# Performance work log

Hardware: AMD Instinct MI355X
Metric: run time of the kernel (lower is better)

Reference implementation:

```python
import jax, jax.numpy as jnp
import numpy as np
import math

D_MODEL = 1024
N_HEADS = 16
D_FF = 4096
D_K = D_MODEL // N_HEADS
B, S = 2, 2048
EPS = 1e-5


def _linear_params(key, fan_in, fan_out):
    kw, kb = jax.random.split(key)
    bound = 1.0 / math.sqrt(fan_in)
    W = jax.random.uniform(kw, (fan_out, fan_in), jnp.float32, -bound, bound)
    b = jax.random.uniform(kb, (fan_out,), jnp.float32, -bound, bound)
    return W, b


def setup_inputs() -> dict:
    key = jax.random.key(0)
    ks = jax.random.split(key, 8)
    x = jax.random.normal(ks[0], (B, S, D_MODEL), jnp.float32)
    # causal mask, broadcast over batch and heads; 0 -> masked
    mask = jnp.tril(jnp.ones((S, S), jnp.int32))[None, None, :, :]
    wq, bq = _linear_params(ks[1], D_MODEL, D_MODEL)
    wk, bk = _linear_params(ks[2], D_MODEL, D_MODEL)
    wv, bv = _linear_params(ks[3], D_MODEL, D_MODEL)
    wo, bo = _linear_params(ks[4], D_MODEL, D_MODEL)
    w1, b1 = _linear_params(ks[5], D_MODEL, D_FF)
    w2, b2 = _linear_params(ks[6], D_FF, D_MODEL)
    g1 = jnp.ones((D_MODEL,), jnp.float32)
    be1 = jnp.zeros((D_MODEL,), jnp.float32)
    g2 = jnp.ones((D_MODEL,), jnp.float32)
    be2 = jnp.zeros((D_MODEL,), jnp.float32)
    return dict(x=x, mask=mask, wq=wq, bq=bq, wk=wk, bk=bk, wv=wv, bv=bv,
                wo=wo, bo=bo, w1=w1, b1=b1, w2=w2, b2=b2,
                g1=g1, be1=be1, g2=g2, be2=be2)


def _layernorm(x, g, b):
    mu = jnp.mean(x, axis=-1, keepdims=True)
    var = jnp.mean(jnp.square(x - mu), axis=-1, keepdims=True)
    return (x - mu) * jax.lax.rsqrt(var + EPS) * g + b


def reference(x, mask, wq, bq, wk, bk, wv, bv, wo, bo, w1, b1, w2, b2, g1, be1, g2, be2):
    Bsz, Sl, _ = x.shape
    def heads(t):  # [B,S,D] -> [B,H,S,d_k]
        return t.reshape(Bsz, Sl, N_HEADS, D_K).transpose(0, 2, 1, 3)
    Q = heads(x @ wq.T + bq)
    K = heads(x @ wk.T + bk)
    V = heads(x @ wv.T + bv)
    scores = jnp.einsum('bhqd,bhkd->bhqk', Q, K) / math.sqrt(D_K)
    scores = jnp.where(mask == 0, jnp.float32(-1e9), scores)
    attn = jax.nn.softmax(scores, axis=-1)
    out = jnp.einsum('bhqk,bhkd->bhqd', attn, V)
    out = out.transpose(0, 2, 1, 3).reshape(Bsz, Sl, D_MODEL)
    attn_out = out @ wo.T + bo
    h = _layernorm(x + attn_out, g1, be1)  # dropout is identity in eval
    ff = jax.nn.relu(h @ w1.T + b1) @ w2.T + b2
    return _layernorm(h + ff, g2, be2)
```

## Files before the change

kernel.cpp:

```cpp
#include <hip/hip_runtime.h>
#include <hip/hip_bf16.h>


using f32x4 = __attribute__((ext_vector_type(4))) float;
using s16x8 = __attribute__((ext_vector_type(8))) short;

constexpr int D_MODEL = 1024;
constexpr int D_FF    = 4096;
constexpr int DK      = 64;
constexpr int BB      = 2;
constexpr int SS      = 2048;
constexpr int NTOK    = BB * SS;

#define QSCALE 0.18033688011112042f

__device__ __forceinline__ ushort f2bf(float f) {
    unsigned u = __float_as_uint(f);
    u += 0x7fffu + ((u >> 16) & 1u);
    return (ushort)(u >> 16);
}

__device__ __forceinline__ float bflo(uint v) { return __uint_as_float(v << 16); }
__device__ __forceinline__ float bfhi(uint v) { return __uint_as_float(v & 0xffff0000u); }

__device__ __forceinline__ float ex2(float x) {
    float r;
    asm("v_exp_f32 %0, %1" : "=v"(r) : "v"(x));
    return r;
}

__device__ __forceinline__ void gload_lds16(const void* g, void* l) {
    __builtin_amdgcn_global_load_lds(
        (const __attribute__((address_space(1))) void*)g,
        (__attribute__((address_space(3))) void*)l, 16, 0, 0);
}

__device__ __forceinline__ void wait_vm4() {
    asm volatile("s_waitcnt vmcnt(4)" ::: "memory");
    __builtin_amdgcn_sched_barrier(0);
}
__device__ __forceinline__ void wait_vm0() {
    asm volatile("s_waitcnt vmcnt(0)" ::: "memory");
    __builtin_amdgcn_sched_barrier(0);
}
__device__ __forceinline__ void wait_lgkm0() {
    asm volatile("s_waitcnt lgkmcnt(0)" ::: "memory");
    __builtin_amdgcn_sched_barrier(0);
}

struct CvtArgs { const float* src[7]; ushort* dst[7]; };

__global__ __launch_bounds__(256) void cvt_all(CvtArgs a) {
    constexpr long S[8] = {0L<<20, 1L<<20, 2L<<20, 3L<<20,
                           4L<<20, 8L<<20, 12L<<20, 16L<<20};
    long i = ((long)blockIdx.x * 256 + threadIdx.x) * 4;
    int s = 0;
#pragma unroll
    for (int j = 1; j < 7; ++j) if (i >= S[j]) s = j;
    long off = i - S[s];
    float4 v = *(const float4*)(a.src[s] + off);
    ushort4 o;
    o.x = f2bf(v.x); o.y = f2bf(v.y); o.z = f2bf(v.z); o.w = f2bf(v.w);
    *(ushort4*)(a.dst[s] + off) = o;
}

__global__ __launch_bounds__(512, 2) void gemm256_relu(
        const ushort* __restrict__ A, const ushort* __restrict__ Wt,
        const float* __restrict__ bias, ushort* __restrict__ C,
        int M, int N, int K) {
    __shared__ __align__(16) char Als[2][2][128 * 128];
    __shared__ __align__(16) char Bls[2][2][128 * 128];

    const int nwg = (int)gridDim.x;
    const int id  = (int)blockIdx.x;
    const int sw  = (id & 7) * (nwg >> 3) + (id >> 3);
    const int gx  = N >> 8;
    const int bx  = sw % gx, by = sw / gx;
    const int bm0 = by << 8, bn0 = bx << 8;

    const int t  = threadIdx.x;
    const int l  = t & 63;
    const int w  = t >> 6;
    const int li = l & 15, g = l >> 4;
    const int wm = w >> 2, wn = w & 3;

    const int srow  = w * 8 + (l >> 3);
    const int scolb = (l & 7) * 16;
    const int svz   = (scolb ^ ((srow & 4) << 3)) >> 1;
    const int nk    = K >> 6;

    auto stA = [&](int buf, int half, int kt) {
        if (kt >= nk) return;
        const ushort* src = A + (size_t)(bm0 + half * 128 + srow) * K + kt * 64 + svz;
        char* dst = Als[buf][half] + w * 1024;
        gload_lds16(src, dst);
        gload_lds16(src + (size_t)64 * K, dst + 8192);
    };
    auto stB = [&](int buf, int half, int kt) {
        if (kt >= nk) return;
        const ushort* src = Wt + (size_t)(bn0 + half * 128 + srow) * K + kt * 64 + svz;
        char* dst = Bls[buf][half] + w * 1024;
        gload_lds16(src, dst);
        gload_lds16(src + (size_t)64 * K, dst + 8192);
    };

    const int rdsw = (li & 4) << 3;

    f32x4 acc[8][4];
#pragma unroll
    for (int m = 0; m < 8; ++m)
#pragma unroll
        for (int n = 0; n < 4; ++n)
            acc[m][n] = (f32x4){0.f, 0.f, 0.f, 0.f};

    auto ldA2 = [&](int buf, int q, s16x8 af[2][2]) {
#pragma unroll
        for (int m2 = 0; m2 < 2; ++m2)
#pragma unroll
            for (int kk = 0; kk < 2; ++kk)
                af[m2][kk] = *(const s16x8*)(Als[buf][wm] +
                    ((q * 2 + m2) * 16 + li) * 128 + ((kk * 64 + g * 16) ^ rdsw));
    };
    auto ldB8 = [&](int buf, s16x8 bfr[4][2]) {
#pragma unroll
        for (int nf = 0; nf < 4; ++nf)
#pragma unroll
            for (int kk = 0; kk < 2; ++kk)
                bfr[nf][kk] = *(const s16x8*)(Bls[buf][wn >> 1] +
                    ((wn & 1) * 64 + nf * 16 + li) * 128 + ((kk * 64 + g * 16) ^ rdsw));
    };
    auto mfmaq = [&](int q, s16x8 af[2][2], s16x8 bfr[4][2], int wm_mode) {
        __builtin_amdgcn_s_barrier();
        wait_lgkm0();
        __builtin_amdgcn_s_setprio(1);
#pragma unroll
        for (int m2 = 0; m2 < 2; ++m2)
#pragma unroll
            for (int nf = 0; nf < 4; ++nf)
#pragma unroll
            for (int kk = 0; kk < 2; ++kk)
                acc[q * 2 + m2][nf] = __builtin_amdgcn_mfma_f32_16x16x32_bf16(
                    af[m2][kk], bfr[nf][kk], acc[q * 2 + m2][nf], 0, 0, 0);
        __builtin_amdgcn_s_setprio(0);
        if (wm_mode == 4) wait_vm4();
        else if (wm_mode == 0) wait_vm0();
        __builtin_amdgcn_s_barrier();
    };

    stB(0, 0, 0); stB(0, 1, 0);
    stA(0, 0, 0); stA(0, 1, 0);
    stB(1, 0, 1); stB(1, 1, 1);
    wait_vm4();
    __builtin_amdgcn_s_barrier();

    const int ni = nk >> 1;
    for (int i = 0; i < ni; ++i) {
        const int t0 = 2 * i;
        const bool last = (i == ni - 1);
        {
            s16x8 bfr[4][2];
            { ldB8(0, bfr); s16x8 af[2][2]; ldA2(0, 0, af);
              stA(1, 0, t0 + 1);                      mfmaq(0, af, bfr, -1); }
            { s16x8 af[2][2]; ldA2(0, 1, af);
              stA(1, 1, t0 + 1); stB(0, 0, t0 + 2);   mfmaq(1, af, bfr, -1); }
            { s16x8 af[2][2]; ldA2(0, 2, af);
              stB(0, 1, t0 + 2);                      mfmaq(2, af, bfr, -1); }
            { s16x8 af[2][2]; ldA2(0, 3, af);
                                                      mfmaq(3, af, bfr, last ? 0 : 4); }
        }
        {
            s16x8 bfr[4][2];
            { ldB8(1, bfr); s16x8 af[2][2]; ldA2(1, 0, af);
              stA(0, 0, t0 + 2);                      mfmaq(0, af, bfr, -1); }
            { s16x8 af[2][2]; ldA2(1, 1, af);
              stA(0, 1, t0 + 2);                      mfmaq(1, af, bfr, -1); }
            { s16x8 af[2][2]; ldA2(1, 2, af);
              stB(1, 0, t0 + 3);                      mfmaq(2, af, bfr, -1); }
            { s16x8 af[2][2]; ldA2(1, 3, af);
              stB(1, 1, t0 + 3);
                                                      mfmaq(3, af, bfr, last ? -1 : 4); }
        }
    }

#pragma unroll
    for (int mf = 0; mf < 8; ++mf) {
        int row0 = bm0 + wm * 128 + mf * 16 + g * 4;
#pragma unroll
        for (int nf = 0; nf < 4; ++nf) {
            int col = bn0 + wn * 64 + nf * 16 + li;
            float bsv = bias[col];
#pragma unroll
            for (int r = 0; r < 4; ++r) {
                float v = fmaxf(acc[mf][nf][r] + bsv, 0.f);
                C[(size_t)(row0 + r) * N + col] = f2bf(v);
            }
        }
    }
}

template <bool RELU, bool OUTBF16>
__global__ __launch_bounds__(256, 2) void gemm_bt(
        const ushort* __restrict__ A, const ushort* __restrict__ W,
        const float* __restrict__ bias,
        void* __restrict__ Cout, int M, int N, int Klen, int ldk, int gx, int splitk) {
    __shared__ __align__(16) char Asb[2][128 * 128];
    __shared__ __align__(16) char Bsb[2][128 * 128];

    const int nwg = (int)gridDim.x;
    const int id  = (int)blockIdx.x;
    const int sw  = (id & 7) * (nwg >> 3) + (id >> 3);
    const int tps = nwg / splitk;
    const int s   = sw / tps;
    const int rem = sw - s * tps;
    const int bx  = rem % gx, by = rem / gx;

    const int t  = threadIdx.x;
    const int l  = t & 63;
    const int w  = t >> 6;
    const int wr = w >> 1, wc = w & 1;
    const int li = l & 15, g = l >> 4;
    const int bm0 = by << 7;
    const int bn0 = bx << 7;
    const int kbase = s * Klen;

    f32x4 acc[4][4];
#pragma unroll
    for (int m = 0; m < 4; ++m)
#pragma unroll
        for (int n = 0; n < 4; ++n)
            acc[m][n] = (f32x4){0.f, 0.f, 0.f, 0.f};

    const int rsub = l >> 3, slot = l & 7;
    const int swzel = (((slot * 16) ^ (rsub << 4)) >> 1);

    auto stage = [&](int buf, int k0) {
#pragma unroll
        for (int i = 0; i < 4; ++i) {
            const int rbase = i * 32 + w * 8;
            gload_lds16(A + (size_t)(bm0 + rbase + rsub) * ldk + kbase + k0 + swzel,
                        Asb[buf] + rbase * 128);
            gload_lds16(W + (size_t)(bn0 + rbase + rsub) * ldk + kbase + k0 + swzel,
                        Bsb[buf] + rbase * 128);
        }
    };

    const int nk = Klen >> 6;
    stage(0, 0);
    __syncthreads();

    for (int tt = 0; tt < nk; ++tt) {
        const int cur = tt & 1;
        if (tt + 1 < nk) stage(cur ^ 1, (tt + 1) << 6);
#pragma unroll
        for (int ks = 0; ks < 2; ++ks) {
            s16x8 af[4], bfr[4];
#pragma unroll
            for (int m = 0; m < 4; ++m) {
                int row = wr * 64 + m * 16 + li;
                af[m] = *(const s16x8*)(Asb[cur] + row * 128 + (((ks * 4 + g) * 16) ^ ((row & 7) << 4)));
            }
#pragma unroll
            for (int n = 0; n < 4; ++n) {
                int row = wc * 64 + n * 16 + li;
                bfr[n] = *(const s16x8*)(Bsb[cur] + row * 128 + (((ks * 4 + g) * 16) ^ ((row & 7) << 4)));
            }
            __builtin_amdgcn_s_setprio(1);
#pragma unroll
            for (int m = 0; m < 4; ++m)
#pragma unroll
                for (int n = 0; n < 4; ++n)
                    acc[m][n] = __builtin_amdgcn_mfma_f32_16x16x32_bf16(af[m], bfr[n], acc[m][n], 0, 0, 0);
            __builtin_amdgcn_s_setprio(0);
        }
        __syncthreads();
    }

    const bool dobias = (s == 0);
    float* Cf = (float*)Cout + (size_t)s * M * N;
#pragma unroll
    for (int m = 0; m < 4; ++m) {
        int row0 = bm0 + wr * 64 + m * 16 + g * 4;
#pragma unroll
        for (int n = 0; n < 4; ++n) {
            int col = bn0 + wc * 64 + n * 16 + li;
            float bsv = dobias ? bias[col] : 0.f;
#pragma unroll
            for (int r = 0; r < 4; ++r) {
                float v = acc[m][n][r] + bsv;
                if (RELU) v = fmaxf(v, 0.f);
                size_t idx = (size_t)(row0 + r) * N + col;
                if (OUTBF16) ((ushort*)Cout)[idx] = f2bf(v);
                else         Cf[idx] = v;
            }
        }
    }
}

__global__ __launch_bounds__(256, 2) void gemm_qkvt(
        const ushort* __restrict__ xb, const ushort* __restrict__ wqkb,
        const ushort* __restrict__ wvb,
        const float* __restrict__ bq, const float* __restrict__ bk,
        const float* __restrict__ bv,
        ushort* __restrict__ QKb, ushort* __restrict__ VtG) {
    __shared__ __align__(16) char Asb[2][128 * 128];
    __shared__ __align__(16) char Bsb[2][128 * 128];

    const int id = (int)blockIdx.x;
    const int sw = (id & 7) * 96 + (id >> 3);
    const bool vt = (sw >= 512);
    int bx, by, N;
    const ushort *A, *W;
    if (!vt) { bx = sw % 16;          by = sw / 16;          A = xb;  W = wqkb; N = 2048; }
    else     { int s2 = sw - 512; bx = s2 % 32; by = s2 / 32; A = wvb; W = xb;  N = 4096; }

    const int t  = threadIdx.x;
    const int l  = t & 63;
    const int w  = t >> 6;
    const int wr = w >> 1, wc = w & 1;
    const int li = l & 15, g = l >> 4;
    const int bm0 = by << 7;
    const int bn0 = bx << 7;

    f32x4 acc[4][4];
#pragma unroll
    for (int m = 0; m < 4; ++m)
#pragma unroll
        for (int n = 0; n < 4; ++n)
            acc[m][n] = (f32x4){0.f, 0.f, 0.f, 0.f};

    const int rsub = l >> 3, slot = l & 7;
    const int swzel = (((slot * 16) ^ (rsub << 4)) >> 1);

    auto stage = [&](int buf, int k0) {
#pragma unroll
        for (int i = 0; i < 4; ++i) {
            const int rbase = i * 32 + w * 8;
            gload_lds16(A + (size_t)(bm0 + rbase + rsub) * 1024 + k0 + swzel,
                        Asb[buf] + rbase * 128);
            gload_lds16(W + (size_t)(bn0 + rbase + rsub) * 1024 + k0 + swzel,
                        Bsb[buf] + rbase * 128);
        }
    };

    stage(0, 0);
    __syncthreads();

    for (int tt = 0; tt < 16; ++tt) {
        const int cur = tt & 1;
        if (tt + 1 < 16) stage(cur ^ 1, (tt + 1) << 6);
#pragma unroll
        for (int ks = 0; ks < 2; ++ks) {
            s16x8 af[4], bfr[4];
#pragma unroll
            for (int m = 0; m < 4; ++m) {
                int row = wr * 64 + m * 16 + li;
                af[m] = *(const s16x8*)(Asb[cur] + row * 128 + (((ks * 4 + g) * 16) ^ ((row & 7) << 4)));
            }
#pragma unroll
            for (int n = 0; n < 4; ++n) {
                int row = wc * 64 + n * 16 + li;
                bfr[n] = *(const s16x8*)(Bsb[cur] + row * 128 + (((ks * 4 + g) * 16) ^ ((row & 7) << 4)));
            }
            __builtin_amdgcn_s_setprio(1);
#pragma unroll
            for (int m = 0; m < 4; ++m)
#pragma unroll
                for (int n = 0; n < 4; ++n)
                    acc[m][n] = __builtin_amdgcn_mfma_f32_16x16x32_bf16(af[m], bfr[n], acc[m][n], 0, 0, 0);
            __builtin_amdgcn_s_setprio(0);
        }
        __syncthreads();
    }

#pragma unroll
    for (int m = 0; m < 4; ++m) {
        int row0 = bm0 + wr * 64 + m * 16 + g * 4;
#pragma unroll
        for (int n = 0; n < 4; ++n) {
            int col = bn0 + wc * 64 + n * 16 + li;
            if (!vt) {
                float bsv = (col < 1024) ? bq[col] : bk[col - 1024];
                float sc  = (col < 1024) ? QSCALE : 1.f;
#pragma unroll
                for (int r = 0; r < 4; ++r) {
                    float v = (acc[m][n][r] + bsv) * sc;
                    QKb[(size_t)(row0 + r) * 2048 + col] = f2bf(v);
                }
            } else {
#pragma unroll
                for (int r = 0; r < 4; ++r) {
                    float v = acc[m][n][r] + bv[row0 + r];
                    VtG[(size_t)(row0 + r) * 4096 + col] = f2bf(v);
                }
            }
        }
    }
}

__global__ __launch_bounds__(256, 4) void attn_kernel(
        const ushort* __restrict__ QKb, const ushort* __restrict__ VtG,
        ushort* __restrict__ po, float* __restrict__ ml) {
    __shared__ __align__(16) char Ks[2][64 * 128];
    __shared__ __align__(16) char Vs[2][64 * 128];
    __shared__ __align__(16) char Ps[4][16 * 128];

    const int t  = threadIdx.x;
    const int l  = t & 63;
    const int w  = t >> 6;
    const int li = l & 15, g = l >> 4;

    const int id   = (int)blockIdx.x;
    const int xcd  = id & 7;
    const int rest = id >> 3;
    const int grp  = xcd + 8 * (rest >> 5);
    const int k32  = rest & 31;
    const int h    = grp >> 1;
    const int b    = grp & 1;
    const int bx   = k32 & 15;
    const int half = k32 >> 4;

    const ushort* Kp = QKb + (size_t)(b * SS) * 2048 + 1024 + h * DK;
    const ushort* Vp = VtG + (size_t)(h * DK) * NTOK + b * SS;

    const int rsub = l >> 3, slot = l & 7;
    const int swzsrc = (slot * 16) ^ (rsub << 4);

    auto stage = [&](int buf, int kt) {
#pragma unroll
        for (int c = 0; c < 2; ++c) {
            int row0 = (w + c * 4) * 8;
            gload_lds16((const char*)(Kp + (size_t)(kt + row0 + rsub) * 2048) + swzsrc,
                        Ks[buf] + row0 * 128);
            gload_lds16((const char*)(Vp + (size_t)(row0 + rsub) * NTOK + kt) + swzsrc,
                        Vs[buf] + row0 * 128);
        }
    };

    char* Pw = Ps[w];
    const int rswz = (li & 7) << 4;

    const int hi  = SS / 64 - 1 - bx;
    const int lo  = bx;
    const int qwH = hi * 64 + w * 16;
    const int qwL = lo * 64 + w * 16;

    s16x8 qfH[2], qfL[2];
    {
        const ushort* QpH = QKb + (size_t)(b * SS + qwH) * 2048 + h * DK;
        const ushort* QpL = QKb + (size_t)(b * SS + qwL) * 2048 + h * DK;
#pragma unroll
        for (int ds = 0; ds < 2; ++ds) {
            qfH[ds] = *(const s16x8*)(QpH + li * 2048 + ds * 32 + g * 8);
            qfL[ds] = *(const s16x8*)(QpL + li * 2048 + ds * 32 + g * 8);
        }
    }

    f32x4 oH[4], oL[4];
#pragma unroll
    for (int d = 0; d < 4; ++d) {
        oH[d] = (f32x4){0.f, 0.f, 0.f, 0.f};
        oL[d] = (f32x4){0.f, 0.f, 0.f, 0.f};
    }
    float mH = -1e30f, lsH = 0.f, mL = -1e30f, lsL = 0.f;

    auto process = [&](const s16x8 (&qf)[2], f32x4 (&o)[4], float& m_, float& ls,
                       int j, int stripe, int qw, int cur) {
        const int kt = j * 64;
        f32x4 sa[4];
#pragma unroll
        for (int ks = 0; ks < 4; ++ks) sa[ks] = (f32x4){0.f, 0.f, 0.f, 0.f};
#pragma unroll
        for (int ks = 0; ks < 4; ++ks) {
            int row = ks * 16 + li;
#pragma unroll
            for (int ds = 0; ds < 2; ++ds) {
                s16x8 kf = *(const s16x8*)(Ks[cur] + row * 128 + ((ds * 64 + g * 16) ^ rswz));
                __builtin_amdgcn_s_setprio(1);
                sa[ks] = __builtin_amdgcn_mfma_f32_16x16x32_bf16(kf, qf[ds], sa[ks], 0, 0, 0);
                __builtin_amdgcn_s_setprio(0);
            }
        }

        const bool maskt = (j == stripe);
        float p[4][4];
        float pmax = -1e30f;
#pragma unroll
        for (int ks = 0; ks < 4; ++ks)
#pragma unroll
            for (int r = 0; r < 4; ++r) {
                float sv = sa[ks][r];
                if (maskt && (kt + ks * 16 + g * 4 + r > qw + li)) sv = -1e30f;
                p[ks][r] = sv;
                pmax = fmaxf(pmax, sv);
            }

        if (!__all(pmax <= m_ + 11.5f)) {
            float mx = fmaxf(pmax, __shfl_xor(pmax, 16));
            mx = fmaxf(mx, __shfl_xor(mx, 32));
            float nm = fmaxf(m_, mx);
            float fs = ex2(m_ - nm);
            m_ = nm;
            ls *= fs;
            float fsr[4];
#pragma unroll
            for (int r = 0; r < 4; ++r) fsr[r] = __shfl(fs, g * 4 + r);
#pragma unroll
            for (int d = 0; d < 4; ++d)
#pragma unroll
                for (int r = 0; r < 4; ++r) o[d][r] *= fsr[r];
        }
        float rs = 0.f;
#pragma unroll
        for (int ks = 0; ks < 4; ++ks)
#pragma unroll
            for (int r = 0; r < 4; ++r) {
                p[ks][r] = ex2(p[ks][r] - m_);
                rs += p[ks][r];
            }
        rs += __shfl_xor(rs, 16);
        rs += __shfl_xor(rs, 32);
        ls += rs;

#pragma unroll
        for (int ks = 0; ks < 4; ++ks) {
            uint u0, u1;
            asm("v_cvt_pk_bf16_f32 %0, %1, %2" : "=v"(u0) : "v"(p[ks][0]), "v"(p[ks][1]));
            asm("v_cvt_pk_bf16_f32 %0, %1, %2" : "=v"(u1) : "v"(p[ks][2]), "v"(p[ks][3]));
            uint2 uv; uv.x = u0; uv.y = u1;
            *(uint2*)(Pw + li * 128 + ((ks * 32 + g * 8) ^ rswz)) = uv;
        }

        s16x8 pf[2];
#pragma unroll
        for (int ks2 = 0; ks2 < 2; ++ks2)
            pf[ks2] = *(const s16x8*)(Pw + li * 128 + ((ks2 * 64 + g * 16) ^ rswz));
#pragma unroll
        for (int dblk = 0; dblk < 4; ++dblk) {
            int vrow = dblk * 16 + li;
#pragma unroll
            for (int ks2 = 0; ks2 < 2; ++ks2) {
                s16x8 vf = *(const s16x8*)(Vs[cur] + vrow * 128 + ((ks2 * 64 + g * 16) ^ rswz));
                __builtin_amdgcn_s_setprio(1);
                o[dblk] = __builtin_amdgcn_mfma_f32_16x16x32_bf16(pf[ks2], vf, o[dblk], 0, 0, 0);
                __builtin_amdgcn_s_setprio(0);
            }
        }
    };

    const int nt = ((hi - half) >> 1) + 1;
    stage(0, half * 64);
    __syncthreads();

    for (int it = 0; it < nt; ++it) {
        const int j   = half + 2 * it;
        const int cur = it & 1;
        if (it + 1 < nt) stage(cur ^ 1, j * 64 + 128);

        process(qfH, oH, mH, lsH, j, hi, qwH, cur);
        if (j <= lo)
            process(qfL, oL, mL, lsL, j, lo, qwL, cur);

        __syncthreads();
    }

#pragma unroll
    for (int r = 0; r < 4; ++r) {
        ushort* ppH = po + ((((size_t)(half * 2 + b)) * SS + qwH + g * 4 + r) * 16 + h) * 64;
        ushort* ppL = po + ((((size_t)(half * 2 + b)) * SS + qwL + g * 4 + r) * 16 + h) * 64;
#pragma unroll
        for (int dblk = 0; dblk < 4; ++dblk) {
            ppH[dblk * 16 + li] = f2bf(oH[dblk][r]);
            ppL[dblk * 16 + li] = f2bf(oL[dblk][r]);
        }
    }
    if (l < 16) {
        size_t mrowH = (((size_t)(half * 2 + b)) * SS + qwH + l) * 16 + h;
        ml[mrowH * 2]     = mH;
        ml[mrowH * 2 + 1] = lsH;
        size_t mrowL = (((size_t)(half * 2 + b)) * SS + qwL + l) * 16 + h;
        ml[mrowL * 2]     = mL;
        ml[mrowL * 2 + 1] = lsL;
    }
}

__global__ __launch_bounds__(256) void attn_combine(
        const ushort* __restrict__ po, const float* __restrict__ ml,
        ushort* __restrict__ ctx) {
    const int idx = blockIdx.x * 256 + threadIdx.x;
    const int row = idx >> 4;
    const int d4  = (idx & 15) * 4;
    const int HR  = 2 * SS * 16;

    float m0 = ml[(size_t)row * 2],        l0 = ml[(size_t)row * 2 + 1];
    float m1 = ml[(size_t)(HR + row) * 2], l1 = ml[(size_t)(HR + row) * 2 + 1];
    float mx = fmaxf(m0, m1);
    float w0 = ex2(m0 - mx), w1 = ex2(m1 - mx);
    float inv = 1.0f / (l0 * w0 + l1 * w1);

    uint2 a = *(const uint2*)(po + (size_t)row * 64 + d4);
    uint2 c = *(const uint2*)(po + (size_t)(HR + row) * 64 + d4);
    float v0 = (bflo(a.x) * w0 + bflo(c.x) * w1) * inv;
    float v1 = (bfhi(a.x) * w0 + bfhi(c.x) * w1) * inv;
    float v2 = (bflo(a.y) * w0 + bflo(c.y) * w1) * inv;
    float v3 = (bfhi(a.y) * w0 + bfhi(c.y) * w1) * inv;
    ushort4 o;
    o.x = f2bf(v0); o.y = f2bf(v1); o.z = f2bf(v2); o.w = f2bf(v3);
    *(ushort4*)(ctx + (size_t)(row >> 4) * 1024 + (row & 15) * 64 + d4) = o;
}

template <bool WBF, bool X3>
__global__ __launch_bounds__(256) void ln_fused(
        const float* __restrict__ xa, const float* __restrict__ xb,
        const float* __restrict__ xc,
        const float* __restrict__ gamma, const float* __restrict__ beta,
        float* __restrict__ outf, ushort* __restrict__ outb) {
    const int row = blockIdx.x;
    const int t   = threadIdx.x;
    const size_t off = (size_t)row * D_MODEL + t * 4;
    float4 a = *(const float4*)(xa + off);
    float4 c = *(const float4*)(xb + off);
    float z0 = a.x + c.x, z1 = a.y + c.y, z2 = a.z + c.z, z3 = a.w + c.w;
    if constexpr (X3) {
        float4 d = *(const float4*)(xc + off);
        z0 += d.x; z1 += d.y; z2 += d.z; z3 += d.w;
    }
    float sum = z0 + z1 + z2 + z3;
    float sq  = z0 * z0 + z1 * z1 + z2 * z2 + z3 * z3;
#pragma unroll
    for (int o = 1; o < 64; o <<= 1) {
        sum += __shfl_xor(sum, o);
        sq  += __shfl_xor(sq, o);
    }
    __shared__ float s1[4], s2[4];
    if ((t & 63) == 0) { s1[t >> 6] = sum; s2[t >> 6] = sq; }
    __syncthreads();
    float tot = s1[0] + s1[1] + s1[2] + s1[3];
    float tsq = s2[0] + s2[1] + s2[2] + s2[3];
    const float invn = 1.0f / (float)D_MODEL;
    float mu  = tot * invn;
    float var = tsq * invn - mu * mu;
    float rstd = rsqrtf(var + 1e-5f);
    float4 gv = *(const float4*)(gamma + t * 4);
    float4 bv = *(const float4*)(beta + t * 4);
    float y0 = (z0 - mu) * rstd * gv.x + bv.x;
    float y1 = (z1 - mu) * rstd * gv.y + bv.y;
    float y2 = (z2 - mu) * rstd * gv.z + bv.z;
    float y3 = (z3 - mu) * rstd * gv.w + bv.w;
    float4 y = {y0, y1, y2, y3};
    *(float4*)(outf + off) = y;
    if constexpr (WBF) {
        ushort4 u;
        u.x = f2bf(y0); u.y = f2bf(y1); u.z = f2bf(y2); u.w = f2bf(y3);
        *(ushort4*)(outb + off) = u;
    }
}

extern "C" void kernel_launch(void* const* d_in, const int* in_sizes, int n_in,
                              void* d_out, int out_size, void* d_ws, size_t ws_size,
                              hipStream_t stream) {
    const float* x   = (const float*)d_in[0];
    const float* wq  = (const float*)d_in[2];  const float* bq  = (const float*)d_in[3];
    const float* wk  = (const float*)d_in[4];  const float* bk  = (const float*)d_in[5];
    const float* wv  = (const float*)d_in[6];  const float* bv  = (const float*)d_in[7];
    const float* wo  = (const float*)d_in[8];  const float* bo  = (const float*)d_in[9];
    const float* w1  = (const float*)d_in[10]; const float* b1  = (const float*)d_in[11];
    const float* w2  = (const float*)d_in[12]; const float* b2  = (const float*)d_in[13];
    const float* g1  = (const float*)d_in[14]; const float* be1 = (const float*)d_in[15];
    const float* g2  = (const float*)d_in[16]; const float* be2 = (const float*)d_in[17];
    float* out = (float*)d_out;

    char* ws = (char*)d_ws;
    const size_t MB = 1u << 20;
    ushort* wqkb = (ushort*)(ws + 0 * MB);
    ushort* wvb  = (ushort*)(ws + 4 * MB);
    ushort* wob  = (ushort*)(ws + 6 * MB);
    ushort* w1b  = (ushort*)(ws + 8 * MB);
    ushort* w2b  = (ushort*)(ws + 16 * MB);
    ushort* xb   = (ushort*)(ws + 24 * MB);
    ushort* QKb  = (ushort*)(ws + 32 * MB);
    ushort* VtG  = (ushort*)(ws + 48 * MB);
    ushort* ctx  = (ushort*)(ws + 56 * MB);
    ushort* po   = (ushort*)(ws + 64 * MB);
    float*  ml   = (float*)(ws + 81 * MB);
    float*  p0   = (float*)(ws + 64 * MB);
    float*  p1   = (float*)(ws + 80 * MB);
    float*  h    = (float*)(ws + 96 * MB);
    ushort* hb   = (ushort*)(ws + 112 * MB);
    ushort* ffib = (ushort*)(ws + 24 * MB);

    CvtArgs ca;
    ca.src[0] = wq; ca.dst[0] = wqkb;
    ca.src[1] = wk; ca.dst[1] = wqkb + D_MODEL * D_MODEL;
    ca.src[2] = wv; ca.dst[2] = wvb;
    ca.src[3] = wo; ca.dst[3] = wob;
    ca.src[4] = w1; ca.dst[4] = w1b;
    ca.src[5] = w2; ca.dst[5] = w2b;
    ca.src[6] = x;  ca.dst[6] = xb;
    cvt_all<<<dim3(16384), dim3(256), 0, stream>>>(ca);

    dim3 blk(256);
    gemm_qkvt<<<dim3(768), blk, 0, stream>>>(xb, wqkb, wvb, bq, bk, bv, QKb, VtG);

    attn_kernel<<<dim3(1024), blk, 0, stream>>>(QKb, VtG, po, ml);
    attn_combine<<<dim3(4096), blk, 0, stream>>>(po, ml, ctx);

    gemm_bt<false, false><<<dim3(512), blk, 0, stream>>>(
        ctx, wob, bo, p0, NTOK, D_MODEL, 512, D_MODEL, 8, 2);
    ln_fused<true, true><<<dim3(NTOK), blk, 0, stream>>>(x, p0, p1, g1, be1, h, hb);

    gemm256_relu<<<dim3(256), dim3(512), 0, stream>>>(hb, w1b, b1, ffib, NTOK, D_FF, D_MODEL);

    gemm_bt<false, false><<<dim3(512), blk, 0, stream>>>(
        ffib, w2b, b2, p0, NTOK, D_MODEL, 2048, D_FF, 8, 2);
    ln_fused<false, true><<<dim3(NTOK), blk, 0, stream>>>(h, p0, p1, g2, be2, out, nullptr);
}
```

Before: 229.8 us.

## Replace QKV projection GEMM with 256x256-tile pipelined 8-wave kernel

The fused Q/K/V-transpose projection moves from 128x128 tiles with 4 waves to 256x256 tiles with 8 waves, modeled on the existing gemm256_relu kernel. It uses split half-tile LDS staging with explicit vmcnt/lgkm waits and barriers, which raises per-block data reuse and overlaps global loads with MFMA work. The grid shrinks from 768 to 192 blocks, so on a large-CU device some compute units may sit idle or see uneven load. Register pressure and LDS use per block also go up.

```diff
diff --git a/kernel.cpp b/kernel.cpp
--- a/kernel.cpp
+++ b/kernel.cpp
@@ -198,6 +198,152 @@
     }
 }
 
+__global__ __launch_bounds__(512, 2) void gemm256_qkvt(
+        const ushort* __restrict__ xb, const ushort* __restrict__ wqkb,
+        const ushort* __restrict__ wvb,
+        const float* __restrict__ bq, const float* __restrict__ bk,
+        const float* __restrict__ bv,
+        ushort* __restrict__ QKb, ushort* __restrict__ VtG) {
+    __shared__ __align__(16) char Als[2][2][128 * 128];
+    __shared__ __align__(16) char Bls[2][2][128 * 128];
+
+    const int id = (int)blockIdx.x;
+    const int sw = (id & 7) * 24 + (id >> 3);
+    const bool vt = (sw >= 128);
+    const ushort *Aop, *Wop;
+    int bm0, bn0;
+    if (!vt) { bm0 = (sw >> 3) << 8;  bn0 = (sw & 7) << 8;          Aop = xb;  Wop = wqkb; }
+    else     { int s2 = sw - 128; bm0 = (s2 >> 4) << 8; bn0 = (s2 & 15) << 8; Aop = wvb; Wop = xb; }
+
+    const int t  = threadIdx.x;
+    const int l  = t & 63;
+    const int w  = t >> 6;
+    const int li = l & 15, g = l >> 4;
+    const int wm = w >> 2, wn = w & 3;
+
+    const int srow  = w * 8 + (l >> 3);
+    const int scolb = (l & 7) * 16;
+    const int svz   = (scolb ^ ((srow & 4) << 3)) >> 1;
+    constexpr int K = 1024, nk = 16;
+
+    auto stA = [&](int buf, int half, int kt) {
+        if (kt >= nk) return;
+        const ushort* src = Aop + (size_t)(bm0 + half * 128 + srow) * K + kt * 64 + svz;
+        char* dst = Als[buf][half] + w * 1024;
+        gload_lds16(src, dst);
+        gload_lds16(src + (size_t)64 * K, dst + 8192);
+    };
+    auto stB = [&](int buf, int half, int kt) {
+        if (kt >= nk) return;
+        const ushort* src = Wop + (size_t)(bn0 + half * 128 + srow) * K + kt * 64 + svz;
+        char* dst = Bls[buf][half] + w * 1024;
+        gload_lds16(src, dst);
+        gload_lds16(src + (size_t)64 * K, dst + 8192);
+    };
+
+    const int rdsw = (li & 4) << 3;
+
+    f32x4 acc[8][4];
+#pragma unroll
+    for (int m = 0; m < 8; ++m)
+#pragma unroll
+        for (int n = 0; n < 4; ++n)
+            acc[m][n] = (f32x4){0.f, 0.f, 0.f, 0.f};
+
+    auto ldA2 = [&](int buf, int q, s16x8 af[2][2]) {
+#pragma unroll
+        for (int m2 = 0; m2 < 2; ++m2)
+#pragma unroll
+            for (int kk = 0; kk < 2; ++kk)
+                af[m2][kk] = *(const s16x8*)(Als[buf][wm] +
+                    ((q * 2 + m2) * 16 + li) * 128 + ((kk * 64 + g * 16) ^ rdsw));
+    };
+    auto ldB8 = [&](int buf, s16x8 bfr[4][2]) {
+#pragma unroll
+        for (int nf = 0; nf < 4; ++nf)
+#pragma unroll
+            for (int kk = 0; kk < 2; ++kk)
+                bfr[nf][kk] = *(const s16x8*)(Bls[buf][wn >> 1] +
+                    ((wn & 1) * 64 + nf * 16 + li) * 128 + ((kk * 64 + g * 16) ^ rdsw));
+    };
+    auto mfmaq = [&](int q, s16x8 af[2][2], s16x8 bfr[4][2], int wm_mode) {
+        __builtin_amdgcn_s_barrier();
+        wait_lgkm0();
+        __builtin_amdgcn_s_setprio(1);
+#pragma unroll
+        for (int m2 = 0; m2 < 2; ++m2)
+#pragma unroll
+            for (int nf = 0; nf < 4; ++nf)
+#pragma unroll
+            for (int kk = 0; kk < 2; ++kk)
+                acc[q * 2 + m2][nf] = __builtin_amdgcn_mfma_f32_16x16x32_bf16(
+                    af[m2][kk], bfr[nf][kk], acc[q * 2 + m2][nf], 0, 0, 0);
+        __builtin_amdgcn_s_setprio(0);
+        if (wm_mode == 4) wait_vm4();
+        else if (wm_mode == 0) wait_vm0();
+        __builtin_amdgcn_s_barrier();
+    };
+
+    stB(0, 0, 0); stB(0, 1, 0);
+    stA(0, 0, 0); stA(0, 1, 0);
+    stB(1, 0, 1); stB(1, 1, 1);
+    wait_vm4();
+    __builtin_amdgcn_s_barrier();
+
+    const int ni = nk >> 1;
+    for (int i = 0; i < ni; ++i) {
+        const int t0 = 2 * i;
+        const bool last = (i == ni - 1);
+        {
+            s16x8 bfr[4][2];
+            { ldB8(0, bfr); s16x8 af[2][2]; ldA2(0, 0, af);
+              stA(1, 0, t0 + 1);                      mfmaq(0, af, bfr, -1); }
+            { s16x8 af[2][2]; ldA2(0, 1, af);
+              stA(1, 1, t0 + 1); stB(0, 0, t0 + 2);   mfmaq(1, af, bfr, -1); }
+            { s16x8 af[2][2]; ldA2(0, 2, af);
+              stB(0, 1, t0 + 2);                      mfmaq(2, af, bfr, -1); }
+            { s16x8 af[2][2]; ldA2(0, 3, af);
+                                                      mfmaq(3, af, bfr, last ? 0 : 4); }
+        }
+        {
+            s16x8 bfr[4][2];
+            { ldB8(1, bfr); s16x8 af[2][2]; ldA2(1, 0, af);
+              stA(0, 0, t0 + 2);                      mfmaq(0, af, bfr, -1); }
+            { s16x8 af[2][2]; ldA2(1, 1, af);
+              stA(0, 1, t0 + 2);                      mfmaq(1, af, bfr, -1); }
+            { s16x8 af[2][2]; ldA2(1, 2, af);
+              stB(1, 0, t0 + 3);                      mfmaq(2, af, bfr, -1); }
+            { s16x8 af[2][2]; ldA2(1, 3, af);
+              stB(1, 1, t0 + 3);
+                                                      mfmaq(3, af, bfr, last ? -1 : 4); }
+        }
+    }
+
+#pragma unroll
+    for (int mf = 0; mf < 8; ++mf) {
+        int row0 = bm0 + wm * 128 + mf * 16 + g * 4;
+#pragma unroll
+        for (int nf = 0; nf < 4; ++nf) {
+            int col = bn0 + wn * 64 + nf * 16 + li;
+            if (!vt) {
+                float bsv = (col < 1024) ? bq[col] : bk[col - 1024];
+                float sc  = (col < 1024) ? QSCALE : 1.f;
+#pragma unroll
+                for (int r = 0; r < 4; ++r) {
+                    float v = (acc[mf][nf][r] + bsv) * sc;
+                    QKb[(size_t)(row0 + r) * 2048 + col] = f2bf(v);
+                }
+            } else {
+#pragma unroll
+                for (int r = 0; r < 4; ++r) {
+                    float v = acc[mf][nf][r] + bv[row0 + r];
+                    VtG[(size_t)(row0 + r) * 4096 + col] = f2bf(v);
+                }
+            }
+        }
+    }
+}
+
 template <bool RELU, bool OUTBF16>
 __global__ __launch_bounds__(256, 2) void gemm_bt(
         const ushort* __restrict__ A, const ushort* __restrict__ W,
@@ -291,107 +437,6 @@
                 size_t idx = (size_t)(row0 + r) * N + col;
                 if (OUTBF16) ((ushort*)Cout)[idx] = f2bf(v);
                 else         Cf[idx] = v;
-            }
-        }
-    }
-}
-
-__global__ __launch_bounds__(256, 2) void gemm_qkvt(
-        const ushort* __restrict__ xb, const ushort* __restrict__ wqkb,
-        const ushort* __restrict__ wvb,
-        const float* __restrict__ bq, const float* __restrict__ bk,
-        const float* __restrict__ bv,
-        ushort* __restrict__ QKb, ushort* __restrict__ VtG) {
-    __shared__ __align__(16) char Asb[2][128 * 128];
-    __shared__ __align__(16) char Bsb[2][128 * 128];
-
-    const int id = (int)blockIdx.x;
-    const int sw = (id & 7) * 96 + (id >> 3);
-    const bool vt = (sw >= 512);
-    int bx, by, N;
-    const ushort *A, *W;
-    if (!vt) { bx = sw % 16;          by = sw / 16;          A = xb;  W = wqkb; N = 2048; }
-    else     { int s2 = sw - 512; bx = s2 % 32; by = s2 / 32; A = wvb; W = xb;  N = 4096; }
-
-    const int t  = threadIdx.x;
-    const int l  = t & 63;
-    const int w  = t >> 6;
-    const int wr = w >> 1, wc = w & 1;
-    const int li = l & 15, g = l >> 4;
-    const int bm0 = by << 7;
-    const int bn0 = bx << 7;
-
-    f32x4 acc[4][4];
-#pragma unroll
-    for (int m = 0; m < 4; ++m)
-#pragma unroll
-        for (int n = 0; n < 4; ++n)
-            acc[m][n] = (f32x4){0.f, 0.f, 0.f, 0.f};
-
-    const int rsub = l >> 3, slot = l & 7;
-    const int swzel = (((slot * 16) ^ (rsub << 4)) >> 1);
-
-    auto stage = [&](int buf, int k0) {
-#pragma unroll
-        for (int i = 0; i < 4; ++i) {
-            const int rbase = i * 32 + w * 8;
-            gload_lds16(A + (size_t)(bm0 + rbase + rsub) * 1024 + k0 + swzel,
-                        Asb[buf] + rbase * 128);
-            gload_lds16(W + (size_t)(bn0 + rbase + rsub) * 1024 + k0 + swzel,
-                        Bsb[buf] + rbase * 128);
-        }
-    };
-
-    stage(0, 0);
-    __syncthreads();
-
-    for (int tt = 0; tt < 16; ++tt) {
-        const int cur = tt & 1;
-        if (tt + 1 < 16) stage(cur ^ 1, (tt + 1) << 6);
-#pragma unroll
-        for (int ks = 0; ks < 2; ++ks) {
-            s16x8 af[4], bfr[4];
-#pragma unroll
-            for (int m = 0; m < 4; ++m) {
-                int row = wr * 64 + m * 16 + li;
-                af[m] = *(const s16x8*)(Asb[cur] + row * 128 + (((ks * 4 + g) * 16) ^ ((row & 7) << 4)));
-            }
-#pragma unroll
-            for (int n = 0; n < 4; ++n) {
-                int row = wc * 64 + n * 16 + li;
-                bfr[n] = *(const s16x8*)(Bsb[cur] + row * 128 + (((ks * 4 + g) * 16) ^ ((row & 7) << 4)));
-            }
-            __builtin_amdgcn_s_setprio(1);
-#pragma unroll
-            for (int m = 0; m < 4; ++m)
-#pragma unroll
-                for (int n = 0; n < 4; ++n)
-                    acc[m][n] = __builtin_amdgcn_mfma_f32_16x16x32_bf16(af[m], bfr[n], acc[m][n], 0, 0, 0);
-            __builtin_amdgcn_s_setprio(0);
-        }
-        __syncthreads();
-    }
-
-#pragma unroll
-    for (int m = 0; m < 4; ++m) {
-        int row0 = bm0 + wr * 64 + m * 16 + g * 4;
-#pragma unroll
-        for (int n = 0; n < 4; ++n) {
-            int col = bn0 + wc * 64 + n * 16 + li;
-            if (!vt) {
-                float bsv = (col < 1024) ? bq[col] : bk[col - 1024];
-                float sc  = (col < 1024) ? QSCALE : 1.f;
-#pragma unroll
-                for (int r = 0; r < 4; ++r) {
-                    float v = (acc[m][n][r] + bsv) * sc;
-                    QKb[(size_t)(row0 + r) * 2048 + col] = f2bf(v);
-                }
-            } else {
-#pragma unroll
-                for (int r = 0; r < 4; ++r) {
-                    float v = acc[m][n][r] + bv[row0 + r];
-                    VtG[(size_t)(row0 + r) * 4096 + col] = f2bf(v);
-                }
             }
         }
     }
@@ -698,19 +743,19 @@
     ca.src[6] = x;  ca.dst[6] = xb;
     cvt_all<<<dim3(16384), dim3(256), 0, stream>>>(ca);
 
-    dim3 blk(256);
-    gemm_qkvt<<<dim3(768), blk, 0, stream>>>(xb, wqkb, wvb, bq, bk, bv, QKb, VtG);
-
-    attn_kernel<<<dim3(1024), blk, 0, stream>>>(QKb, VtG, po, ml);
-    attn_combine<<<dim3(4096), blk, 0, stream>>>(po, ml, ctx);
-
-    gemm_bt<false, false><<<dim3(512), blk, 0, stream>>>(
+    gemm256_qkvt<<<dim3(192), dim3(512), 0, stream>>>(
+        xb, wqkb, wvb, bq, bk, bv, QKb, VtG);
+
+    attn_kernel<<<dim3(1024), dim3(256), 0, stream>>>(QKb, VtG, po, ml);
+    attn_combine<<<dim3(4096), dim3(256), 0, stream>>>(po, ml, ctx);
+
+    gemm_bt<false, false><<<dim3(512), dim3(256), 0, stream>>>(
         ctx, wob, bo, p0, NTOK, D_MODEL, 512, D_MODEL, 8, 2);
-    ln_fused<true, true><<<dim3(NTOK), blk, 0, stream>>>(x, p0, p1, g1, be1, h, hb);
+    ln_fused<true, true><<<dim3(NTOK), dim3(256), 0, stream>>>(x, p0, p1, g1, be1, h, hb);
 
     gemm256_relu<<<dim3(256), dim3(512), 0, stream>>>(hb, w1b, b1, ffib, NTOK, D_FF, D_MODEL);
 
-    gemm_bt<false, false><<<dim3(512), blk, 0, stream>>>(
+    gemm_bt<false, false><<<dim3(512), dim3(256), 0, stream>>>(
         ffib, w2b, b2, p0, NTOK, D_MODEL, 2048, D_FF, 8, 2);
-    ln_fused<false, true><<<dim3(NTOK), blk, 0, stream>>>(h, p0, p1, g2, be2, out, nullptr);
-}
+    ln_fused<false, true><<<dim3(NTOK), dim3(256), 0, stream>>>(h, p0, p1, g2, be2, out, nullptr);
+}
```

New measurement: 226.6 us. Within noise of the previous version (-1.4%).
